# Kernel tuning notes

Measured on AMD Instinct MI355X. Metric: run time of the kernel, lower is better.

Reference implementation:

```python
import jax, jax.numpy as jnp
import numpy as np

N_PROTO = 16

def setup_inputs() -> dict:
    key = jax.random.key(0)
    k1, k2 = jax.random.split(key)
    x = jax.random.normal(k1, (1, 200000, 768), dtype=jnp.float32)
    prototypes = jax.random.normal(k2, (N_PROTO, 768), dtype=jnp.float32)
    return {"x": x, "prototypes": prototypes}


def reference(x, prototypes):
    # Row-normalize prototypes (done once in __init__ in the torch module)
    protos = prototypes / jnp.linalg.norm(prototypes, axis=1, keepdims=True)  # [P, D]
    # L2-normalize patch embeddings: x / ||x||
    xn = x / jnp.linalg.norm(x, axis=-1, keepdims=True)                        # [1, N, D]
    x0 = xn[0]                                                                  # [N, D]
    # cdist(protos, xn) with unit-norm rows: d^2 = 2 - 2 * <p, x>
    sim = protos @ x0.T                                                         # [P, N]
    dist = jnp.sqrt(jnp.maximum(2.0 - 2.0 * sim, 0.0))
    assign = jnp.argmin(dist, axis=0)                                           # [N] int
    # Per-prototype mean pooling (fused scatter-mean instead of python loop)
    sums = jax.ops.segment_sum(x0, assign, num_segments=N_PROTO)                # [P, D]
    counts = jax.ops.segment_sum(jnp.ones((x0.shape[0],), x0.dtype), assign,
                                 num_segments=N_PROTO)[:, None]                 # [P, 1]
    means = jnp.where(counts > 0, sums / jnp.maximum(counts, 1.0), 0.0)         # [P, D]
    out = means.reshape(1, -1)                                                  # [1, P*D]
    return out
```

## Files before the change

kernel.cpp:

```cpp
#include <hip/hip_runtime.h>

#define NP 16
#define D 768
#define NBLK 512
#define NTHR 256
#define RPI 32
#define DSL 192
#define NM 12


typedef short short8 __attribute__((ext_vector_type(8)));
typedef float f32x4 __attribute__((ext_vector_type(4)));
typedef unsigned u32x2 __attribute__((ext_vector_type(2)));

#define LDS_OFF(ptr) ((unsigned)(size_t)(__attribute__((address_space(3))) const void*)(ptr))

static __device__ __forceinline__ unsigned f2bf_u(float f) {
    unsigned u = __float_as_uint(f);
    u += 0x7FFF + ((u >> 16) & 1);
    return u >> 16;
}
static __device__ __forceinline__ unsigned pack2bf(float lo, float hi) {
    return f2bf_u(lo) | (f2bf_u(hi) << 16);
}

__global__ __launch_bounds__(64) void setup_kernel(const float* __restrict__ protos,
                                                   float* __restrict__ ws) {
    const int p = blockIdx.x, lane = threadIdx.x;
    const float* pr = protos + p * D;
    float v[12];
    float ns = 0.f;
#pragma unroll
    for (int j = 0; j < 12; ++j) {
        v[j] = pr[lane + 64 * j];
        ns = fmaf(v[j], v[j], ns);
    }
#pragma unroll
    for (int m = 1; m < 64; m <<= 1) ns += __shfl_xor(ns, m);
    const float rn = 1.0f / sqrtf(ns);
    unsigned short* ptf = (unsigned short*)ws;
#pragma unroll
    for (int j = 0; j < 12; ++j) {
        const int c = lane + 64 * j;
        const int s = c >> 5, sub = c & 31, g = sub >> 3, jj = sub & 7;
        ptf[(unsigned)((s * 64 + g * 16 + p) * 8 + jj)] = (unsigned short)f2bf_u(v[j] * rn);
    }
}

__global__ __launch_bounds__(NTHR, 2) void fused_kernel(const float* __restrict__ x,
                                                        const float* __restrict__ ws,
                                                        float* __restrict__ gpart,
                                                        float* __restrict__ gcnt,
                                                        int nrows, int niter) {
    __shared__ short8 sPT[24 * 64];
    __shared__ unsigned short tileT[24576];
    __shared__ f32x4 simred[2][64];
    __shared__ float normred[2][16];
    __shared__ float rS[RPI];
    __shared__ int aS[RPI];
    __shared__ float C[NP];

    const int tid = threadIdx.x, w = tid >> 6, lane = tid & 63;
    const int r15 = lane & 15, g = lane >> 4;
    const int tp = w >> 1, h = w & 1;

    {
        const uint4* src = (const uint4*)ws;
        uint4* dst = (uint4*)sPT;
        for (int i = tid; i < 1536; i += NTHR) dst[i] = src[i];
    }
    if (tid < NP) C[tid] = 0.f;
    __syncthreads();

    f32x4 acc[NM];
#pragma unroll
    for (int m = 0; m < NM; ++m) acc[m] = (f32x4){0.f, 0.f, 0.f, 0.f};

    for (int it = blockIdx.x; it < niter; it += NBLK) {
        const int rb = it * RPI;
        const int base = rb + tp * 16;

        const int rowc = min(base + r15, nrows - 1);
        const float* xr = x + (size_t)rowc * D + h * 384 + (g << 3);
        const short8* bp = sPT + lane;
        f32x4 sa = {0.f, 0.f, 0.f, 0.f};
        float nse = 0.f, nso = 0.f;
        const unsigned q = (unsigned)(tp * 4 + (r15 >> 2));
        const unsigned rr = (unsigned)(r15 & 3);
        const unsigned cc0 = (unsigned)((g & 1) * 8);
#pragma unroll
        for (int s = 0; s < 12; ++s) {
            const float4 f0 = *(const float4*)(xr + s * 32);
            const float4 f1 = *(const float4*)(xr + s * 32 + 4);
            nse = fmaf(f0.x, f0.x, fmaf(f0.y, f0.y, fmaf(f0.z, f0.z, fmaf(f0.w, f0.w, nse))));
            nso = fmaf(f1.x, f1.x, fmaf(f1.y, f1.y, fmaf(f1.z, f1.z, fmaf(f1.w, f1.w, nso))));
            uint4 au;
            au.x = pack2bf(f0.x, f0.y);
            au.y = pack2bf(f0.z, f0.w);
            au.z = pack2bf(f1.x, f1.y);
            au.w = pack2bf(f1.z, f1.w);
            const unsigned cb = (unsigned)(h * 24 + s * 2 + (g >> 1));
            *(uint4*)&tileT[((q * 48 + cb) * 4 + rr) * 16 + cc0] = au;
            sa = __builtin_amdgcn_mfma_f32_16x16x32_bf16(
                __builtin_bit_cast(short8, au), bp[(h * 12 + s) * 64], sa, 0, 0, 0);
        }
        float ns = nse + nso;
        ns += __shfl_xor(ns, 16);
        ns += __shfl_xor(ns, 32);
        if (h == 1) {
            simred[tp][lane] = sa;
            if (lane < 16) normred[tp][lane] = ns;
        }
        __syncthreads();

        if (h == 0) {
            const f32x4 o = simred[tp][lane];
            f32x4 sc;
#pragma unroll
            for (int r = 0; r < 4; ++r) sc[r] = sa[r] + o[r];
            ns += normred[tp][r15];
            const float rn = 1.0f / sqrtf(ns);
            int ar[4];
#pragma unroll
            for (int r = 0; r < 4; ++r) {
                float bv = sc[r];
                int bi = r15;
#pragma unroll
                for (int m = 1; m <= 8; m <<= 1) {
                    const float ov = __shfl_xor(bv, m);
                    const int oi = __shfl_xor(bi, m);
                    if (ov > bv || (ov == bv && oi < bi)) { bv = ov; bi = oi; }
                }
                ar[r] = bi;
            }
            if (r15 == 0) {
#pragma unroll
                for (int r = 0; r < 4; ++r) {
                    aS[tp * 16 + g * 4 + r] = ar[r];
                    if (base + g * 4 + r < nrows) atomicAdd(&C[ar[r]], 1.0f);
                }
            }
            if (lane < 16) rS[tp * 16 + lane] = (base + lane < nrows) ? rn : 0.f;
        }
        __syncthreads();

        {
            const int nb = g << 3;
            unsigned hb[8];
#pragma unroll
            for (int j = 0; j < 8; ++j) {
                const int an = aS[nb + j];
                const unsigned rb16 = f2bf_u(rS[nb + j]);
                hb[j] = (an == r15) ? rb16 : 0u;
            }
            uint4 au;
            au.x = hb[0] | (hb[1] << 16);
            au.y = hb[2] | (hb[3] << 16);
            au.z = hb[4] | (hb[5] << 16);
            au.w = hb[6] | (hb[7] << 16);
            const short8 afrag = __builtin_bit_cast(short8, au);
            const unsigned qb = (unsigned)(g * 2);
#pragma unroll
            for (int m = 0; m < NM; ++m) {
                const unsigned cb = (unsigned)(w * 12 + m);
                const unsigned a0 =
                    LDS_OFF(&tileT[((qb + 0) * 48 + cb) * 64 + (unsigned)r15 * 4]);
                const unsigned a1 =
                    LDS_OFF(&tileT[((qb + 1) * 48 + cb) * 64 + (unsigned)r15 * 4]);
                u32x2 t0, t1;
                asm volatile("ds_read_b64_tr_b16 %0, %2\n\t"
                             "ds_read_b64_tr_b16 %1, %3\n\t"
                             "s_waitcnt lgkmcnt(0)"
                             : "=&v"(t0), "=&v"(t1)
                             : "v"(a0), "v"(a1));
                uint4 bu;
                bu.x = t0[0]; bu.y = t0[1]; bu.z = t1[0]; bu.w = t1[1];
                acc[m] = __builtin_amdgcn_mfma_f32_16x16x32_bf16(
                    afrag, __builtin_bit_cast(short8, bu), acc[m], 0, 0, 0);
            }
        }
        __syncthreads();
    }

    float* gp = gpart + (size_t)blockIdx.x * (NP * D);
#pragma unroll
    for (int m = 0; m < NM; ++m)
#pragma unroll
        for (int r = 0; r < 4; ++r)
            gp[(g * 4 + r) * D + w * DSL + m * 16 + r15] = acc[m][r];
    if (tid < NP) gcnt[blockIdx.x * NP + tid] = C[tid];
}

__global__ __launch_bounds__(256) void finalize_kernel(const float* __restrict__ gpart,
                                                       const float* __restrict__ gcnt,
                                                       float* __restrict__ out) {
    __shared__ float cnt[NP];
    const int tid = threadIdx.x;
    if (tid < NP) {
        float c = 0.f;
        for (int b = 0; b < NBLK; ++b) c += gcnt[b * NP + tid];
        cnt[tid] = c;
    }
    __syncthreads();
    const int i = blockIdx.x * 256 + tid;
    if (i < NP * D) {
        float s = 0.f;
#pragma unroll 8
        for (int b = 0; b < NBLK; ++b) s += gpart[(size_t)b * (NP * D) + i];
        const float c = cnt[i / D];
        out[i] = (c > 0.f) ? s / fmaxf(c, 1.0f) : 0.f;
    }
}

extern "C" void kernel_launch(void* const* d_in, const int* in_sizes, int n_in,
                              void* d_out, int out_size, void* d_ws, size_t ws_size,
                              hipStream_t stream) {
    const float* x = (const float*)d_in[0];
    const float* protos = (const float*)d_in[1];
    float* ws = (float*)d_ws;
    float* out = (float*)d_out;
    const int nrows = in_sizes[0] / D;
    const int niter = (nrows + RPI - 1) / RPI;

    float* gpart = ws + 6144;
    float* gcnt = ws + 6144 + (size_t)NBLK * (NP * D);

    setup_kernel<<<16, 64, 0, stream>>>(protos, ws);
    fused_kernel<<<NBLK, NTHR, 0, stream>>>(x, ws, gpart, gcnt, nrows, niter);
    finalize_kernel<<<(NP * D + 255) / 256, 256, 0, stream>>>(gpart, gcnt, out);
}
```

Baseline: 156.4 us.

## Reduce block partials with global atomics and batch transposed LDS reads

Each block now atomically adds its per-prototype sums and counts into one zero-initialised global buffer, which setup_kernel clears. Before, every block wrote a full partial slab that finalize_kernel then read back in a 512-way reduction. The pooling loop also issues eight ds_read_b64_tr_b16 loads per wait instead of two, so fewer s_waitcnt stalls sit between MFMAs. The cost is contention on 12K float atomics per block and a summation order that is no longer deterministic.

```diff
diff --git a/kernel.cpp b/kernel.cpp
--- a/kernel.cpp
+++ b/kernel.cpp
@@ -27,6 +27,10 @@
 __global__ __launch_bounds__(64) void setup_kernel(const float* __restrict__ protos,
                                                    float* __restrict__ ws) {
     const int p = blockIdx.x, lane = threadIdx.x;
+    float* gsum = ws + 6144 + p * D;
+    for (int j = lane; j < D; j += 64) gsum[j] = 0.f;
+    if (lane == 0) ws[18432 + p] = 0.f;
+
     const float* pr = protos + p * D;
     float v[12];
     float ns = 0.f;
@@ -49,7 +53,7 @@
 
 __global__ __launch_bounds__(NTHR, 2) void fused_kernel(const float* __restrict__ x,
                                                         const float* __restrict__ ws,
-                                                        float* __restrict__ gpart,
+                                                        float* __restrict__ gsum,
                                                         float* __restrict__ gcnt,
                                                         int nrows, int niter) {
     __shared__ short8 sPT[24 * 64];
@@ -160,54 +164,63 @@
             au.w = hb[6] | (hb[7] << 16);
             const short8 afrag = __builtin_bit_cast(short8, au);
             const unsigned qb = (unsigned)(g * 2);
-#pragma unroll
-            for (int m = 0; m < NM; ++m) {
-                const unsigned cb = (unsigned)(w * 12 + m);
-                const unsigned a0 =
-                    LDS_OFF(&tileT[((qb + 0) * 48 + cb) * 64 + (unsigned)r15 * 4]);
-                const unsigned a1 =
-                    LDS_OFF(&tileT[((qb + 1) * 48 + cb) * 64 + (unsigned)r15 * 4]);
-                u32x2 t0, t1;
-                asm volatile("ds_read_b64_tr_b16 %0, %2\n\t"
-                             "ds_read_b64_tr_b16 %1, %3\n\t"
-                             "s_waitcnt lgkmcnt(0)"
-                             : "=&v"(t0), "=&v"(t1)
-                             : "v"(a0), "v"(a1));
-                uint4 bu;
-                bu.x = t0[0]; bu.y = t0[1]; bu.z = t1[0]; bu.w = t1[1];
-                acc[m] = __builtin_amdgcn_mfma_f32_16x16x32_bf16(
-                    afrag, __builtin_bit_cast(short8, bu), acc[m], 0, 0, 0);
+            const unsigned lb = (unsigned)r15 * 4;
+#pragma unroll
+            for (int mg = 0; mg < 3; ++mg) {
+                const unsigned cb0 = (unsigned)(w * 12 + mg * 4);
+                u32x2 t[8];
+                unsigned a[8];
+#pragma unroll
+                for (int mm = 0; mm < 4; ++mm) {
+                    a[2 * mm] = LDS_OFF(&tileT[((qb + 0) * 48 + cb0 + mm) * 64 + lb]);
+                    a[2 * mm + 1] = LDS_OFF(&tileT[((qb + 1) * 48 + cb0 + mm) * 64 + lb]);
+                }
+                asm volatile(
+                    "ds_read_b64_tr_b16 %0, %8\n\t"
+                    "ds_read_b64_tr_b16 %1, %9\n\t"
+                    "ds_read_b64_tr_b16 %2, %10\n\t"
+                    "ds_read_b64_tr_b16 %3, %11\n\t"
+                    "ds_read_b64_tr_b16 %4, %12\n\t"
+                    "ds_read_b64_tr_b16 %5, %13\n\t"
+                    "ds_read_b64_tr_b16 %6, %14\n\t"
+                    "ds_read_b64_tr_b16 %7, %15\n\t"
+                    "s_waitcnt lgkmcnt(0)"
+                    : "=&v"(t[0]), "=&v"(t[1]), "=&v"(t[2]), "=&v"(t[3]),
+                      "=&v"(t[4]), "=&v"(t[5]), "=&v"(t[6]), "=&v"(t[7])
+                    : "v"(a[0]), "v"(a[1]), "v"(a[2]), "v"(a[3]),
+                      "v"(a[4]), "v"(a[5]), "v"(a[6]), "v"(a[7]));
+#pragma unroll
+                for (int mm = 0; mm < 4; ++mm) {
+                    uint4 bu;
+                    bu.x = t[2 * mm][0];
+                    bu.y = t[2 * mm][1];
+                    bu.z = t[2 * mm + 1][0];
+                    bu.w = t[2 * mm + 1][1];
+                    acc[mg * 4 + mm] = __builtin_amdgcn_mfma_f32_16x16x32_bf16(
+                        afrag, __builtin_bit_cast(short8, bu), acc[mg * 4 + mm], 0, 0, 0);
+                }
             }
         }
         __syncthreads();
     }
 
-    float* gp = gpart + (size_t)blockIdx.x * (NP * D);
 #pragma unroll
     for (int m = 0; m < NM; ++m)
 #pragma unroll
         for (int r = 0; r < 4; ++r)
-            gp[(g * 4 + r) * D + w * DSL + m * 16 + r15] = acc[m][r];
-    if (tid < NP) gcnt[blockIdx.x * NP + tid] = C[tid];
-}
-
-__global__ __launch_bounds__(256) void finalize_kernel(const float* __restrict__ gpart,
-                                                       const float* __restrict__ gcnt,
+            __hip_atomic_fetch_add(&gsum[(g * 4 + r) * D + w * DSL + m * 16 + r15],
+                                   acc[m][r], __ATOMIC_RELAXED, __HIP_MEMORY_SCOPE_AGENT);
+    if (tid < NP)
+        __hip_atomic_fetch_add(&gcnt[tid], C[tid], __ATOMIC_RELAXED,
+                               __HIP_MEMORY_SCOPE_AGENT);
+}
+
+__global__ __launch_bounds__(256) void finalize_kernel(const float* __restrict__ ws,
                                                        float* __restrict__ out) {
-    __shared__ float cnt[NP];
-    const int tid = threadIdx.x;
-    if (tid < NP) {
-        float c = 0.f;
-        for (int b = 0; b < NBLK; ++b) c += gcnt[b * NP + tid];
-        cnt[tid] = c;
-    }
-    __syncthreads();
-    const int i = blockIdx.x * 256 + tid;
+    const int i = blockIdx.x * 256 + threadIdx.x;
     if (i < NP * D) {
-        float s = 0.f;
-#pragma unroll 8
-        for (int b = 0; b < NBLK; ++b) s += gpart[(size_t)b * (NP * D) + i];
-        const float c = cnt[i / D];
+        const float c = ws[18432 + i / D];
+        const float s = ws[6144 + i];
         out[i] = (c > 0.f) ? s / fmaxf(c, 1.0f) : 0.f;
     }
 }
@@ -222,10 +235,7 @@
     const int nrows = in_sizes[0] / D;
     const int niter = (nrows + RPI - 1) / RPI;
 
-    float* gpart = ws + 6144;
-    float* gcnt = ws + 6144 + (size_t)NBLK * (NP * D);
-
     setup_kernel<<<16, 64, 0, stream>>>(protos, ws);
-    fused_kernel<<<NBLK, NTHR, 0, stream>>>(x, ws, gpart, gcnt, nrows, niter);
-    finalize_kernel<<<(NP * D + 255) / 256, 256, 0, stream>>>(gpart, gcnt, out);
-}
+    fused_kernel<<<NBLK, NTHR, 0, stream>>>(x, ws, ws + 6144, ws + 18432, nrows, niter);
+    finalize_kernel<<<(NP * D + 255) / 256, 256, 0, stream>>>(ws, out);
+}
```

Result: faster. 133.0 us (median of 2 runs) (-15.0%).
